# Performance work log

Hardware: AMD Instinct MI355X
Metric: run time of the kernel (lower is better)

Reference implementation:

```python
import jax, jax.numpy as jnp
import numpy as np

N_NODES = 50000
N_EDGES = 800000
IN_FEAT = 256
OUT_FEAT = 128
P_EDGE = 0.2   # edge dropout rate
P_NODE = 0.1   # node-feature dropout rate
BN_EPS = 1e-5


def setup_inputs() -> dict:
    key = jax.random.key(0)
    ks = jax.random.split(key, 8)
    features = jax.random.normal(ks[0], (N_NODES, IN_FEAT), dtype=jnp.float32)
    W = jax.random.normal(ks[1], (IN_FEAT, OUT_FEAT), dtype=jnp.float32) / np.sqrt(IN_FEAT)
    b = jnp.zeros((OUT_FEAT,), dtype=jnp.float32)
    gamma = jnp.ones((OUT_FEAT,), dtype=jnp.float32)
    beta = jnp.zeros((OUT_FEAT,), dtype=jnp.float32)
    src = jax.random.randint(ks[2], (N_EDGES,), 0, N_NODES, dtype=jnp.int64)
    dst = jax.random.randint(ks[3], (N_EDGES,), 0, N_NODES, dtype=jnp.int64)
    edge_rand = jax.random.uniform(ks[4], (N_EDGES,), dtype=jnp.float32)
    node_rand = jax.random.uniform(ks[5], (N_NODES, OUT_FEAT), dtype=jnp.float32)
    return {"features": features, "W": W, "b": b, "gamma": gamma, "beta": beta,
            "src": src, "dst": dst, "edge_rand": edge_rand, "node_rand": node_rand}


def reference(features, W, b, gamma, beta, src, dst, edge_rand, node_rand):
    dt = features.dtype
    # --- edge dropout: keep-mask over edges (no rescale, per DropEdge convention) ---
    emask = (edge_rand >= P_EDGE).astype(dt)                      # [E]
    # --- GCN conv, norm='both' on the dropped graph ---
    h = features @ W                                              # [N, out] (W first: out < in)
    deg_src = jax.ops.segment_sum(emask, src, num_segments=N_NODES)  # out-degrees
    deg_dst = jax.ops.segment_sum(emask, dst, num_segments=N_NODES)  # in-degrees
    coef = emask * jax.lax.rsqrt(jnp.maximum(deg_src[src], 1.0) * jnp.maximum(deg_dst[dst], 1.0))
    msg = h[src] * coef[:, None]                                  # [E, out]
    agg = jax.ops.segment_sum(msg, dst, num_segments=N_NODES) + b  # [N, out]
    # --- BatchNorm1d (training mode: batch statistics over nodes) ---
    mean = jnp.mean(agg, axis=0)
    var = jnp.var(agg, axis=0)
    y = (agg - mean) * jax.lax.rsqrt(var + BN_EPS) * gamma + beta
    # --- node-feature dropout (inverted scaling) ---
    nmask = (node_rand >= P_NODE).astype(dt) / (1.0 - P_NODE)
    return y * nmask
```

## Files before the change

kernel.cpp:

```cpp
#include <hip/hip_runtime.h>

#define N_NODES 50000
#define N_EDGES 800000
#define IN_FEAT 256
#define OUT_FEAT 128
#define P_EDGE 0.2f
#define P_NODE 0.1f
#define BN_EPS 1e-5f
#define NPART 8
#define CAP_Q 16
#define PART_STRIDE 800000
#define GEMM_BLOCKS 782
#define EDGE_BLOCKS 782
#define EG_BLOCKS 1568
#define ZERO_BLOCKS 782
#define ZERO_CHUNKS 200000
#define PREPW_BLOCKS 128
#define MERGE_BLOCKS 196
#define AGG_BLOCKS 1024
#define FIN_BLOCKS 8

typedef __bf16 bf16x8 __attribute__((ext_vector_type(8)));
typedef float floatx4 __attribute__((ext_vector_type(4)));
typedef float f32x4 __attribute__((ext_vector_type(4)));
typedef int i32x4 __attribute__((ext_vector_type(4)));

__device__ inline float bflo(unsigned u) { return __uint_as_float(u << 16); }
__device__ inline float bfhi(unsigned u) { return __uint_as_float(u & 0xffff0000u); }

__global__ __launch_bounds__(256) void k_init(const float* __restrict__ W,
    uint4* __restrict__ zero_base, __bf16* __restrict__ Wt) {
  if (blockIdx.x < ZERO_BLOCKS) {
    int i = blockIdx.x * 256 + threadIdx.x;
    if (i < ZERO_CHUNKS) zero_base[i] = make_uint4(0u, 0u, 0u, 0u);
  } else {
    int idx = (blockIdx.x - ZERO_BLOCKS) * 256 + threadIdx.x;
    int k = idx >> 7, n = idx & 127;
    Wt[n * IN_FEAT + k] = (__bf16)W[idx];
  }
}

__device__ inline bf16x8 cvt8(f32x4 a, f32x4 b) {
  bf16x8 v;
  v[0] = (__bf16)a[0]; v[1] = (__bf16)a[1]; v[2] = (__bf16)a[2]; v[3] = (__bf16)a[3];
  v[4] = (__bf16)b[0]; v[5] = (__bf16)b[1]; v[6] = (__bf16)b[2]; v[7] = (__bf16)b[3];
  return v;
}

__device__ void edge_body(int ebid, int q,
    const int* __restrict__ src, const int* __restrict__ dst,
    const float* __restrict__ er, unsigned* __restrict__ deg_src_q,
    unsigned* __restrict__ deg_dst_q, unsigned short* __restrict__ parts) {
  unsigned* dsq = deg_src_q + q * N_NODES;
  unsigned* ddq = deg_dst_q + q * N_NODES;
  unsigned short* pq = parts + (size_t)q * PART_STRIDE;
  int t = ebid * 256 + threadIdx.x;
  if (t < N_EDGES / 4) {
    f32x4 e4 = ((const f32x4*)er)[t];
    i32x4 s4 = ((const i32x4*)src)[t];
    i32x4 d4 = ((const i32x4*)dst)[t];
    const bool k0 = e4[0] >= P_EDGE, k1 = e4[1] >= P_EDGE;
    const bool k2 = e4[2] >= P_EDGE, k3 = e4[3] >= P_EDGE;
    unsigned p0 = 0xffffffffu, p1 = 0xffffffffu, p2 = 0xffffffffu, p3 = 0xffffffffu;
    if (k0) p0 = atomicAdd(&ddq[d4[0]], 1u);
    if (k1) p1 = atomicAdd(&ddq[d4[1]], 1u);
    if (k2) p2 = atomicAdd(&ddq[d4[2]], 1u);
    if (k3) p3 = atomicAdd(&ddq[d4[3]], 1u);
    if (k0) atomicAdd(&dsq[s4[0]], 1u);
    if (k1) atomicAdd(&dsq[s4[1]], 1u);
    if (k2) atomicAdd(&dsq[s4[2]], 1u);
    if (k3) atomicAdd(&dsq[s4[3]], 1u);
    if (p0 < CAP_Q) pq[(unsigned)d4[0] * CAP_Q + p0] = (unsigned short)s4[0];
    if (p1 < CAP_Q) pq[(unsigned)d4[1] * CAP_Q + p1] = (unsigned short)s4[1];
    if (p2 < CAP_Q) pq[(unsigned)d4[2] * CAP_Q + p2] = (unsigned short)s4[2];
    if (p3 < CAP_Q) pq[(unsigned)d4[3] * CAP_Q + p3] = (unsigned short)s4[3];
  }
}

__device__ void gemm_body(int bid, const float* __restrict__ feat,
    const __bf16* __restrict__ Wt, __bf16* __restrict__ h) {
  __shared__ char lds[16384];
  const int t = threadIdx.x;
  const int lane = t & 63;
  const int wave = t >> 6;
  const int l16 = lane & 15;
  const int quad = lane >> 4;
  const int m0 = bid * 64 + wave * 16;

  int mload = m0 + l16;
  if (mload >= N_NODES) mload = N_NODES - 1;

  bf16x8 a[8];
#pragma unroll
  for (int kk = 0; kk < 8; kk++) {
    const f32x4* p = (const f32x4*)(feat + (size_t)mload * IN_FEAT + kk * 32 + quad * 8);
    a[kk] = cvt8(p[0], p[1]);
  }

  floatx4 acc[8];
#pragma unroll
  for (int g = 0; g < 8; g++) acc[g] = (floatx4){0.f, 0.f, 0.f, 0.f};

#pragma unroll
  for (int c = 0; c < 4; c++) {
    __syncthreads();
#pragma unroll
    for (int i = 0; i < 4; i++) {
      int ci = i * 256 + t;
      int row = ci >> 3, kseg = ci & 7;
      uint4 v = *(const uint4*)(Wt + (size_t)row * IN_FEAT + c * 64 + kseg * 8);
      *(uint4*)(lds + ((unsigned)(row * 128 + kseg * 16) ^ ((unsigned)(row & 7) << 4))) = v;
    }
    __syncthreads();
#pragma unroll
    for (int g = 0; g < 8; g++) {
      const unsigned row = (unsigned)(g * 16 + l16);
      const unsigned swz = (row & 7u) << 4;
#pragma unroll
      for (int kk = 0; kk < 2; kk++) {
        bf16x8 b = *(const bf16x8*)(lds + ((row * 128u + (unsigned)kk * 64u + (unsigned)quad * 16u) ^ swz));
        acc[g] = __builtin_amdgcn_mfma_f32_16x16x32_bf16(a[c * 2 + kk], b, acc[g], 0, 0, 0);
      }
    }
  }
  __syncthreads();

  char* hb = lds + wave * 4096;
#pragma unroll
  for (int g = 0; g < 8; g++) {
#pragma unroll
    for (int r = 0; r < 4; r++) {
      unsigned row = (unsigned)(quad * 4 + r);
      unsigned o = row * 256u + (unsigned)(g * 16 + l16) * 2u;
      *(__bf16*)(hb + (o ^ ((row & 7u) << 4))) = (__bf16)acc[g][r];
    }
  }
#pragma unroll
  for (int j = 0; j < 4; j++) {
    unsigned row = (unsigned)(lane >> 4) + (unsigned)j * 4u;
    unsigned o = row * 256u + (unsigned)(lane & 15) * 16u;
    uint4 v = *(const uint4*)(hb + (o ^ ((row & 7u) << 4)));
    int grow = m0 + (int)row;
    if (grow < N_NODES)
      *(uint4*)((char*)h + (size_t)grow * 256 + (size_t)(lane & 15) * 16) = v;
  }
}

__global__ __launch_bounds__(256) void k_eg(const float* __restrict__ feat,
    const __bf16* __restrict__ Wt, __bf16* __restrict__ h,
    const int* __restrict__ src, const int* __restrict__ dst,
    const float* __restrict__ er, unsigned* __restrict__ deg_src_q,
    unsigned* __restrict__ deg_dst_q, unsigned short* __restrict__ parts) {
  const int bid = blockIdx.x;
  const int grp = bid >> 3;
  const int l8 = bid & 7;
  const int id = (grp >> 1) * 8 + l8;
  if ((grp & 1) == 0) {
    if (id < EDGE_BLOCKS) edge_body(id, l8, src, dst, er, deg_src_q, deg_dst_q, parts);
  } else {
    if (id < GEMM_BLOCKS) gemm_body(id, feat, Wt, h);
  }
}

__global__ __launch_bounds__(256) void k_merge(const unsigned* __restrict__ deg_src_q,
    const unsigned* __restrict__ deg_dst_q, unsigned long long* __restrict__ cnt8,
    unsigned char* __restrict__ tot8, unsigned char* __restrict__ deg_src_m) {
  int n = blockIdx.x * 256 + threadIdx.x;
  if (n < N_NODES) {
    unsigned ts = 0;
#pragma unroll
    for (int q = 0; q < NPART; q++) ts += deg_src_q[q * N_NODES + n];
    deg_src_m[n] = (unsigned char)(ts > 255u ? 255u : ts);
    unsigned long long pack = 0;
    unsigned tt = 0;
#pragma unroll
    for (int q = 0; q < NPART; q++) {
      unsigned c = deg_dst_q[q * N_NODES + n];
      tt += c;
      c = c > CAP_Q ? CAP_Q : c;
      pack |= (unsigned long long)c << (8 * q);
    }
    cnt8[n] = pack;
    tot8[n] = (unsigned char)(tt > 255u ? 255u : tt);
  }
}

__global__ __launch_bounds__(256) void k_agg(const unsigned short* __restrict__ h,
    const unsigned short* __restrict__ parts, const unsigned char* __restrict__ deg_src_m,
    const unsigned long long* __restrict__ cnt8, const unsigned char* __restrict__ tot8,
    const float* __restrict__ bias, float* __restrict__ out,
    float* __restrict__ psum, float* __restrict__ pssq) {
  const int wid = threadIdx.x >> 6;
  const int lane = threadIdx.x & 63;
  const int g = lane >> 4;
  const int cl = lane & 15;
  const int wave_global = blockIdx.x * 4 + wid;

  float b8[8];
#pragma unroll
  for (int j = 0; j < 8; j++) b8[j] = bias[cl * 8 + j];

  float s8[8], ss8[8];
#pragma unroll
  for (int j = 0; j < 8; j++) { s8[j] = 0.f; ss8[j] = 0.f; }

  for (int d = wave_global; d < N_NODES; d += AGG_BLOCKS * 4) {
    const unsigned long long c8 = cnt8[d];
    unsigned P[8];
    unsigned run = 0;
#pragma unroll
    for (int q = 0; q < 8; q++) { P[q] = run; run += (unsigned)((c8 >> (8 * q)) & 0xffull); }
    const unsigned lim = run;
    const unsigned dbase = (unsigned)d * CAP_Q;

    float acc[8];
#pragma unroll
    for (int j = 0; j < 8; j++) acc[j] = 0.f;

#pragma unroll 2
    for (unsigned i = 0; i < lim; i += 4) {
      unsigned e = i + (unsigned)g;
      bool valid = e < lim;
      unsigned ec = valid ? e : 0u;
      unsigned qq = 0, off = 0;
#pragma unroll
      for (int j = 1; j < 8; j++) {
        bool ge = ec >= P[j];
        qq += ge ? 1u : 0u;
        off = ge ? P[j] : off;
      }
      unsigned idx = (unsigned)parts[(size_t)qq * PART_STRIDE + dbase + (ec - off)];
      unsigned dg = deg_src_m[idx];
      float r = valid ? rsqrtf((float)(dg ? dg : 1u)) : 0.f;
      uint4 u = *(const uint4*)(h + (size_t)idx * OUT_FEAT + cl * 8);
      acc[0] = fmaf(bflo(u.x), r, acc[0]);
      acc[1] = fmaf(bfhi(u.x), r, acc[1]);
      acc[2] = fmaf(bflo(u.y), r, acc[2]);
      acc[3] = fmaf(bfhi(u.y), r, acc[3]);
      acc[4] = fmaf(bflo(u.z), r, acc[4]);
      acc[5] = fmaf(bfhi(u.z), r, acc[5]);
      acc[6] = fmaf(bflo(u.w), r, acc[6]);
      acc[7] = fmaf(bfhi(u.w), r, acc[7]);
    }
#pragma unroll
    for (int j = 0; j < 8; j++) {
      acc[j] += __shfl_xor(acc[j], 16);
      acc[j] += __shfl_xor(acc[j], 32);
    }
    if (g == 0) {
      unsigned tot = tot8[d];
      float sc = rsqrtf((float)(tot ? tot : 1u));
      float o[8];
#pragma unroll
      for (int j = 0; j < 8; j++) {
        o[j] = fmaf(acc[j], sc, b8[j]);
        s8[j] += o[j];
        ss8[j] = fmaf(o[j], o[j], ss8[j]);
      }
      float4 o0 = make_float4(o[0], o[1], o[2], o[3]);
      float4 o1 = make_float4(o[4], o[5], o[6], o[7]);
      *(float4*)(out + (size_t)d * OUT_FEAT + cl * 8) = o0;
      *(float4*)(out + (size_t)d * OUT_FEAT + cl * 8 + 4) = o1;
    }
  }

  __shared__ float ls[4][16][8], lss[4][16][8];
  if (g == 0) {
#pragma unroll
    for (int j = 0; j < 8; j++) { ls[wid][cl][j] = s8[j]; lss[wid][cl][j] = ss8[j]; }
  }
  __syncthreads();
  if (threadIdx.x < 128) {
    int pcl = threadIdx.x >> 3, pj = threadIdx.x & 7;
    float t = ls[0][pcl][pj] + ls[1][pcl][pj] + ls[2][pcl][pj] + ls[3][pcl][pj];
    float t2 = lss[0][pcl][pj] + lss[1][pcl][pj] + lss[2][pcl][pj] + lss[3][pcl][pj];
    psum[blockIdx.x * OUT_FEAT + threadIdx.x] = t;
    pssq[blockIdx.x * OUT_FEAT + threadIdx.x] = t2;
  }
}

__global__ __launch_bounds__(256) void k_fin(const float* __restrict__ psum,
    const float* __restrict__ pssq, const float* __restrict__ gamma,
    const float* __restrict__ beta, float* __restrict__ a_coef,
    float* __restrict__ b_coef) {
  const int col16 = threadIdx.x & 15;
  const int slice = threadIdx.x >> 4;
  const int c = blockIdx.x * 16 + col16;
  float t = 0.f, t2 = 0.f;
  for (int b = slice; b < AGG_BLOCKS; b += 16) {
    t += psum[b * OUT_FEAT + c];
    t2 += pssq[b * OUT_FEAT + c];
  }
  __shared__ float S[16][17], S2[16][17];
  S[slice][col16] = t;
  S2[slice][col16] = t2;
  __syncthreads();
  if (threadIdx.x < 16) {
    float ts = 0.f, tss = 0.f;
#pragma unroll
    for (int s = 0; s < 16; s++) { ts += S[s][threadIdx.x]; tss += S2[s][threadIdx.x]; }
    int cc = blockIdx.x * 16 + threadIdx.x;
    float mean = ts * (1.0f / N_NODES);
    float var = tss * (1.0f / N_NODES) - mean * mean;
    float a = gamma[cc] * rsqrtf(var + BN_EPS);
    a_coef[cc] = a;
    b_coef[cc] = fmaf(-mean, a, beta[cc]);
  }
}

__global__ __launch_bounds__(256) void k_norm(float* __restrict__ out,
    const float* __restrict__ node_rand, const float* __restrict__ a_coef,
    const float* __restrict__ b_coef) {
  const size_t total4 = (size_t)N_NODES * OUT_FEAT / 4;
  size_t i = (size_t)blockIdx.x * 256 + threadIdx.x;
  if (i < total4) {
    int c0 = (int)((i * 4) & 127);
    f32x4 v = ((const f32x4*)out)[i];
    f32x4 nr = ((const f32x4*)node_rand)[i];
    f32x4 a = *(const f32x4*)(a_coef + c0);
    f32x4 b = *(const f32x4*)(b_coef + c0);
    const float inv = 1.0f / (1.0f - P_NODE);
    f32x4 o;
    o[0] = (nr[0] >= P_NODE ? inv : 0.f) * fmaf(v[0], a[0], b[0]);
    o[1] = (nr[1] >= P_NODE ? inv : 0.f) * fmaf(v[1], a[1], b[1]);
    o[2] = (nr[2] >= P_NODE ? inv : 0.f) * fmaf(v[2], a[2], b[2]);
    o[3] = (nr[3] >= P_NODE ? inv : 0.f) * fmaf(v[3], a[3], b[3]);
    ((f32x4*)out)[i] = o;
  }
}

extern "C" void kernel_launch(void* const* d_in, const int* in_sizes, int n_in,
                              void* d_out, int out_size, void* d_ws, size_t ws_size,
                              hipStream_t stream) {
  const float* feat  = (const float*)d_in[0];
  const float* W     = (const float*)d_in[1];
  const float* bias  = (const float*)d_in[2];
  const float* gamma = (const float*)d_in[3];
  const float* beta  = (const float*)d_in[4];
  const int*   src   = (const int*)d_in[5];
  const int*   dst   = (const int*)d_in[6];
  const float* er    = (const float*)d_in[7];
  const float* nr    = (const float*)d_in[8];
  float* out = (float*)d_out;

  char* ws = (char*)d_ws;
  __bf16*             h         = (__bf16*)            (ws + 0);
  unsigned short*     parts     = (unsigned short*)    (ws + 12800000);
  __bf16*             Wt        = (__bf16*)            (ws + 25600000);
  unsigned*           deg_src_q = (unsigned*)          (ws + 25665536);
  unsigned*           deg_dst_q = (unsigned*)          (ws + 27265536);
  unsigned long long* cnt8      = (unsigned long long*)(ws + 28865536);
  unsigned char*      tot8      = (unsigned char*)     (ws + 29265536);
  unsigned char*      deg_src_m = (unsigned char*)     (ws + 29315584);
  float*              psum      = (float*)             (ws + 29365760);
  float*              pssq      = (float*)             (ws + 29890048);
  float*              a_coef    = (float*)             (ws + 30414336);
  float*              b_coef    = (float*)             (ws + 30414848);

  k_init<<<ZERO_BLOCKS + PREPW_BLOCKS, 256, 0, stream>>>(
      W, (uint4*)(ws + 25665536), Wt);
  k_eg<<<EG_BLOCKS, 256, 0, stream>>>(feat, Wt, h, src, dst, er,
      deg_src_q, deg_dst_q, parts);
  k_merge<<<MERGE_BLOCKS, 256, 0, stream>>>(deg_src_q, deg_dst_q, cnt8, tot8, deg_src_m);
  k_agg<<<AGG_BLOCKS, 256, 0, stream>>>((const unsigned short*)h, parts,
      deg_src_m, cnt8, tot8, bias, out, psum, pssq);
  k_fin<<<FIN_BLOCKS, 256, 0, stream>>>(psum, pssq, gamma, beta, a_coef, b_coef);
  k_norm<<<(N_NODES * OUT_FEAT / 4 + 255) / 256, 256, 0, stream>>>(out, nr, a_coef, b_coef);
}
```

Measured before the change: 259.9 us.

## Fold BN finalize into norm kernel via atomic 8-way partial sums

After: 238.8 us. 1.09x faster.

```diff
diff --git a/kernel.cpp b/kernel.cpp
--- a/kernel.cpp
+++ b/kernel.cpp
@@ -13,12 +13,11 @@
 #define GEMM_BLOCKS 782
 #define EDGE_BLOCKS 782
 #define EG_BLOCKS 1568
-#define ZERO_BLOCKS 782
-#define ZERO_CHUNKS 200000
+#define ZERO_BLOCKS 784
+#define ZERO_CHUNKS 200512
 #define PREPW_BLOCKS 128
 #define MERGE_BLOCKS 196
-#define AGG_BLOCKS 1024
-#define FIN_BLOCKS 8
+#define AGG_BLOCKS 2048
 
 typedef __bf16 bf16x8 __attribute__((ext_vector_type(8)));
 typedef float floatx4 __attribute__((ext_vector_type(4)));
@@ -189,7 +188,7 @@
     const unsigned short* __restrict__ parts, const unsigned char* __restrict__ deg_src_m,
     const unsigned long long* __restrict__ cnt8, const unsigned char* __restrict__ tot8,
     const float* __restrict__ bias, float* __restrict__ out,
-    float* __restrict__ psum, float* __restrict__ pssq) {
+    float* __restrict__ psum8, float* __restrict__ pssq8) {
   const int wid = threadIdx.x >> 6;
   const int lane = threadIdx.x & 63;
   const int g = lane >> 4;
@@ -270,61 +269,48 @@
     for (int j = 0; j < 8; j++) { ls[wid][cl][j] = s8[j]; lss[wid][cl][j] = ss8[j]; }
   }
   __syncthreads();
+  const int xs = (blockIdx.x & 7) * OUT_FEAT;
   if (threadIdx.x < 128) {
     int pcl = threadIdx.x >> 3, pj = threadIdx.x & 7;
     float t = ls[0][pcl][pj] + ls[1][pcl][pj] + ls[2][pcl][pj] + ls[3][pcl][pj];
     float t2 = lss[0][pcl][pj] + lss[1][pcl][pj] + lss[2][pcl][pj] + lss[3][pcl][pj];
-    psum[blockIdx.x * OUT_FEAT + threadIdx.x] = t;
-    pssq[blockIdx.x * OUT_FEAT + threadIdx.x] = t2;
-  }
-}
-
-__global__ __launch_bounds__(256) void k_fin(const float* __restrict__ psum,
-    const float* __restrict__ pssq, const float* __restrict__ gamma,
-    const float* __restrict__ beta, float* __restrict__ a_coef,
-    float* __restrict__ b_coef) {
-  const int col16 = threadIdx.x & 15;
-  const int slice = threadIdx.x >> 4;
-  const int c = blockIdx.x * 16 + col16;
-  float t = 0.f, t2 = 0.f;
-  for (int b = slice; b < AGG_BLOCKS; b += 16) {
-    t += psum[b * OUT_FEAT + c];
-    t2 += pssq[b * OUT_FEAT + c];
-  }
-  __shared__ float S[16][17], S2[16][17];
-  S[slice][col16] = t;
-  S2[slice][col16] = t2;
-  __syncthreads();
-  if (threadIdx.x < 16) {
+    atomicAdd(&psum8[xs + threadIdx.x], t);
+    atomicAdd(&pssq8[xs + threadIdx.x], t2);
+  }
+}
+
+__global__ __launch_bounds__(256) void k_norm(float* __restrict__ out,
+    const float* __restrict__ node_rand, const float* __restrict__ psum8,
+    const float* __restrict__ pssq8, const float* __restrict__ gamma,
+    const float* __restrict__ beta) {
+  __shared__ float a_s[OUT_FEAT], b_s[OUT_FEAT];
+  const int tid = threadIdx.x;
+  if (tid < OUT_FEAT) {
     float ts = 0.f, tss = 0.f;
 #pragma unroll
-    for (int s = 0; s < 16; s++) { ts += S[s][threadIdx.x]; tss += S2[s][threadIdx.x]; }
-    int cc = blockIdx.x * 16 + threadIdx.x;
+    for (int q = 0; q < NPART; q++) {
+      ts += psum8[q * OUT_FEAT + tid];
+      tss += pssq8[q * OUT_FEAT + tid];
+    }
     float mean = ts * (1.0f / N_NODES);
     float var = tss * (1.0f / N_NODES) - mean * mean;
-    float a = gamma[cc] * rsqrtf(var + BN_EPS);
-    a_coef[cc] = a;
-    b_coef[cc] = fmaf(-mean, a, beta[cc]);
-  }
-}
-
-__global__ __launch_bounds__(256) void k_norm(float* __restrict__ out,
-    const float* __restrict__ node_rand, const float* __restrict__ a_coef,
-    const float* __restrict__ b_coef) {
+    float a = gamma[tid] * rsqrtf(var + BN_EPS);
+    a_s[tid] = a;
+    b_s[tid] = fmaf(-mean, a, beta[tid]);
+  }
+  __syncthreads();
   const size_t total4 = (size_t)N_NODES * OUT_FEAT / 4;
-  size_t i = (size_t)blockIdx.x * 256 + threadIdx.x;
+  size_t i = (size_t)blockIdx.x * 256 + tid;
   if (i < total4) {
     int c0 = (int)((i * 4) & 127);
     f32x4 v = ((const f32x4*)out)[i];
     f32x4 nr = ((const f32x4*)node_rand)[i];
-    f32x4 a = *(const f32x4*)(a_coef + c0);
-    f32x4 b = *(const f32x4*)(b_coef + c0);
     const float inv = 1.0f / (1.0f - P_NODE);
     f32x4 o;
-    o[0] = (nr[0] >= P_NODE ? inv : 0.f) * fmaf(v[0], a[0], b[0]);
-    o[1] = (nr[1] >= P_NODE ? inv : 0.f) * fmaf(v[1], a[1], b[1]);
-    o[2] = (nr[2] >= P_NODE ? inv : 0.f) * fmaf(v[2], a[2], b[2]);
-    o[3] = (nr[3] >= P_NODE ? inv : 0.f) * fmaf(v[3], a[3], b[3]);
+    o[0] = (nr[0] >= P_NODE ? inv : 0.f) * fmaf(v[0], a_s[c0 + 0], b_s[c0 + 0]);
+    o[1] = (nr[1] >= P_NODE ? inv : 0.f) * fmaf(v[1], a_s[c0 + 1], b_s[c0 + 1]);
+    o[2] = (nr[2] >= P_NODE ? inv : 0.f) * fmaf(v[2], a_s[c0 + 2], b_s[c0 + 2]);
+    o[3] = (nr[3] >= P_NODE ? inv : 0.f) * fmaf(v[3], a_s[c0 + 3], b_s[c0 + 3]);
     ((f32x4*)out)[i] = o;
   }
 }
@@ -349,13 +335,11 @@
   __bf16*             Wt        = (__bf16*)            (ws + 25600000);
   unsigned*           deg_src_q = (unsigned*)          (ws + 25665536);
   unsigned*           deg_dst_q = (unsigned*)          (ws + 27265536);
-  unsigned long long* cnt8      = (unsigned long long*)(ws + 28865536);
-  unsigned char*      tot8      = (unsigned char*)     (ws + 29265536);
-  unsigned char*      deg_src_m = (unsigned char*)     (ws + 29315584);
-  float*              psum      = (float*)             (ws + 29365760);
-  float*              pssq      = (float*)             (ws + 29890048);
-  float*              a_coef    = (float*)             (ws + 30414336);
-  float*              b_coef    = (float*)             (ws + 30414848);
+  float*              psum8     = (float*)             (ws + 28865536);
+  float*              pssq8     = (float*)             (ws + 28869632);
+  unsigned long long* cnt8      = (unsigned long long*)(ws + 28873728);
+  unsigned char*      tot8      = (unsigned char*)     (ws + 29273728);
+  unsigned char*      deg_src_m = (unsigned char*)     (ws + 29323776);
 
   k_init<<<ZERO_BLOCKS + PREPW_BLOCKS, 256, 0, stream>>>(
       W, (uint4*)(ws + 25665536), Wt);
@@ -363,7 +347,7 @@
       deg_src_q, deg_dst_q, parts);
   k_merge<<<MERGE_BLOCKS, 256, 0, stream>>>(deg_src_q, deg_dst_q, cnt8, tot8, deg_src_m);
   k_agg<<<AGG_BLOCKS, 256, 0, stream>>>((const unsigned short*)h, parts,
-      deg_src_m, cnt8, tot8, bias, out, psum, pssq);
-  k_fin<<<FIN_BLOCKS, 256, 0, stream>>>(psum, pssq, gamma, beta, a_coef, b_coef);
-  k_norm<<<(N_NODES * OUT_FEAT / 4 + 255) / 256, 256, 0, stream>>>(out, nr, a_coef, b_coef);
-}
+      deg_src_m, cnt8, tot8, bias, out, psum8, pssq8);
+  k_norm<<<(N_NODES * OUT_FEAT / 4 + 255) / 256, 256, 0, stream>>>(
+      out, nr, psum8, pssq8, gamma, beta);
+}
```
